# Kernel tuning notes

Measured on AMD Instinct MI355X. Metric: run time of the kernel, lower is better.

The kernel has to match this reference:

```python
import jax, jax.numpy as jnp
import numpy as np

N_NODES = 100000
HIDDEN = 128
N_ARCS = 1000000


def setup_inputs() -> dict:
    key = jax.random.key(0)
    k1, k2, k3, k4 = jax.random.split(key, 4)
    z = jax.random.normal(k1, (N_NODES, HIDDEN), dtype=jnp.float32)
    pot_arcs = jax.random.randint(k2, (N_ARCS, 2), 0, N_NODES, dtype=jnp.int64)
    # nn.Linear(2H, H): weight [H, 2H], bias [H]
    W1 = jax.random.normal(k3, (HIDDEN, 2 * HIDDEN), dtype=jnp.float32) * (1.0 / np.sqrt(2 * HIDDEN))
    b1 = jnp.zeros((HIDDEN,), dtype=jnp.float32)
    # nn.Linear(H, 1): weight [1, H], bias [1]
    W2 = jax.random.normal(k4, (1, HIDDEN), dtype=jnp.float32) * (1.0 / np.sqrt(HIDDEN))
    b2 = jnp.zeros((1,), dtype=jnp.float32)
    return {"z": z, "pot_arcs": pot_arcs, "W1": W1, "b1": b1, "W2": W2, "b2": b2}


def reference(z, pot_arcs, W1, b1, W2, b2):
    # Gather endpoint embeddings and concat: [E, 2H]
    h = jnp.concatenate([z[pot_arcs[:, 0]], z[pot_arcs[:, 1]]], axis=-1)
    h = jax.nn.relu(h @ W1.T + b1)        # [E, H]
    out = h @ W2.T + b2                   # [E, 1]
    return out.reshape(-1)                # [E]
```

## Files before the change

### kernel.cpp

```cpp
#include <hip/hip_runtime.h>
#include <hip/hip_bf16.h>

#define N_NODES 100000
#define NODES_PAD 100096
#define N_ARCS 1000000

typedef __attribute__((ext_vector_type(8))) short bf16x8;
typedef __attribute__((ext_vector_type(4))) float f32x4;

__device__ __forceinline__ unsigned pk2(float lo, float hi) {
    __hip_bfloat162 b = __float22bfloat162_rn(make_float2(lo, hi));
    union { __hip_bfloat162 b; unsigned u; } c; c.b = b; return c.u;
}

__device__ __forceinline__ uint4 pack8(const float4 a, const float4 b) {
    uint4 r;
    r.x = pk2(a.x, a.y);
    r.y = pk2(a.z, a.w);
    r.z = pk2(b.x, b.y);
    r.w = pk2(b.z, b.w);
    return r;
}

__global__ __launch_bounds__(256) void gemm_uv_q(const float* __restrict__ z,
                                                 const float* __restrict__ W1,
                                                 const float* __restrict__ b1,
                                                 unsigned char* __restrict__ UVq,
                                                 float* __restrict__ scl) {
    __shared__ unsigned short As[64 * 128];
    __shared__ unsigned short Bs[128 * 128];
    const int tid = threadIdx.x;
    const int y = blockIdx.y;
    const int c0 = y * 128;

    #pragma unroll
    for (int it = 0; it < 8; it++) {
        int i = tid + it * 256;
        int row = i >> 4, g = i & 15;
        const float4* s = (const float4*)(W1 + (long)row * 256 + c0 + g * 8);
        ((uint4*)Bs)[row * 16 + (g ^ (row & 15))] = pack8(s[0], s[1]);
    }

    const int lane = tid & 63;
    const int wave = tid >> 6;
    const int l16 = lane & 15;
    const int quad = lane >> 4;

    float bias[8];
    #pragma unroll
    for (int nt = 0; nt < 8; nt++)
        bias[nt] = (y == 0) ? b1[nt * 16 + l16] : 0.0f;

    float* sclh = scl + (long)y * NODES_PAD;

    for (int m0 = blockIdx.x * 64; m0 < N_NODES; m0 += gridDim.x * 64) {
        #pragma unroll
        for (int it = 0; it < 4; it++) {
            int i = tid + it * 256;
            int row = i >> 4, g = i & 15;
            int node = m0 + row;
            uint4 p = make_uint4(0u, 0u, 0u, 0u);
            if (node < N_NODES) {
                const float4* s = (const float4*)(z + (long)node * 128 + g * 8);
                p = pack8(s[0], s[1]);
            }
            ((uint4*)As)[row * 16 + (g ^ (row & 15))] = p;
        }
        __syncthreads();

        const int arow = wave * 16 + l16;
        f32x4 acc[8] = {};
        #pragma unroll
        for (int ks = 0; ks < 4; ks++) {
            const int gb = ks * 4 + quad;
            const bf16x8 a = *(const bf16x8*)&As[arow * 128 + ((gb ^ l16) << 3)];
            #pragma unroll
            for (int nt = 0; nt < 8; nt++) {
                const bf16x8 b = *(const bf16x8*)&Bs[(nt * 16 + l16) * 128 + ((gb ^ l16) << 3)];
                acc[nt] = __builtin_amdgcn_mfma_f32_16x16x32_bf16(a, b, acc[nt], 0, 0, 0);
            }
        }

        float m[4] = {0.f, 0.f, 0.f, 0.f};
        #pragma unroll
        for (int nt = 0; nt < 8; nt++)
            #pragma unroll
            for (int r = 0; r < 4; r++) {
                acc[nt][r] += bias[nt];
                m[r] = fmaxf(m[r], fabsf(acc[nt][r]));
            }
        #pragma unroll
        for (int o = 1; o <= 8; o <<= 1)
            #pragma unroll
            for (int r = 0; r < 4; r++)
                m[r] = fmaxf(m[r], __shfl_xor(m[r], o));

        const int rbase = m0 + wave * 16 + quad * 4;
        float inv[4];
        #pragma unroll
        for (int r = 0; r < 4; r++) {
            m[r] = fmaxf(m[r], 1e-30f);
            inv[r] = 127.0f * __builtin_amdgcn_rcpf(m[r]);
        }
        if (l16 == 0)
            *(float4*)(sclh + rbase) = make_float4(m[0] * (1.f / 127.f), m[1] * (1.f / 127.f),
                                                   m[2] * (1.f / 127.f), m[3] * (1.f / 127.f));
        #pragma unroll
        for (int r = 0; r < 4; r++) {
            unsigned lo = 0, hi = 0;
            #pragma unroll
            for (int nt = 0; nt < 4; nt++) {
                unsigned q = (unsigned)__float2int_rn(fmaf(acc[nt][r], inv[r], 128.f));
                lo |= (q & 0xffu) << (8 * nt);
            }
            #pragma unroll
            for (int nt = 4; nt < 8; nt++) {
                unsigned q = (unsigned)__float2int_rn(fmaf(acc[nt][r], inv[r], 128.f));
                hi |= (q & 0xffu) << (8 * (nt - 4));
            }
            *(uint2*)(UVq + (long)(rbase + r) * 256 + c0 + l16 * 8) = make_uint2(lo, hi);
        }
        __syncthreads();
    }
}

__global__ __launch_bounds__(256) void arc_score(const int4* __restrict__ arcs4,
                                                 const unsigned char* __restrict__ UVq,
                                                 const float* __restrict__ scl,
                                                 const float* __restrict__ W2,
                                                 const float* __restrict__ b2,
                                                 float* __restrict__ out) {
    const int tid = threadIdx.x;
    const int sub = tid & 7;
    const int gq = blockIdx.x * 32 + (tid >> 3);
    const int eb = sub * 16;

    float w2v[16], w2s = 0.f;
    #pragma unroll
    for (int i = 0; i < 16; i++) {
        int col = ((i & 7) << 4) + (sub << 1) + (i >> 3);
        w2v[i] = W2[col];
        w2s += w2v[i];
    }
    const float b2s = b2[0];
    const float* sclV = scl + NODES_PAD;

    const long stride = (long)gridDim.x * 64;
    const long limp = (long)(N_ARCS - 2) >> 1;

    long a = (long)gq * 2;
    int4 i0 = arcs4[a >> 1];
    uint4 u0 = *(const uint4*)(UVq + (long)i0.x * 256 + eb);
    uint4 v0 = *(const uint4*)(UVq + (long)i0.y * 256 + 128 + eb);
    uint4 u1 = *(const uint4*)(UVq + (long)i0.z * 256 + eb);
    uint4 v1 = *(const uint4*)(UVq + (long)i0.w * 256 + 128 + eb);
    float sU0 = scl[i0.x], sV0 = sclV[i0.y];
    float sU1 = scl[i0.z], sV1 = sclV[i0.w];
    long p1i = (a + stride) >> 1; if (p1i > limp) p1i = limp;
    int4 i1 = arcs4[p1i];

    while (true) {
        const long an = a + stride;
        uint4 nu0 = *(const uint4*)(UVq + (long)i1.x * 256 + eb);
        uint4 nv0 = *(const uint4*)(UVq + (long)i1.y * 256 + 128 + eb);
        uint4 nu1 = *(const uint4*)(UVq + (long)i1.z * 256 + eb);
        uint4 nv1 = *(const uint4*)(UVq + (long)i1.w * 256 + 128 + eb);
        float nsU0 = scl[i1.x], nsV0 = sclV[i1.y];
        float nsU1 = scl[i1.z], nsV1 = sclV[i1.w];
        long p2i = (an + stride) >> 1; if (p2i > limp) p2i = limp;
        int4 i2 = arcs4[p2i];

        const float r0 = sV0 * __builtin_amdgcn_rcpf(sU0);
        const float r1 = sV1 * __builtin_amdgcn_rcpf(sU1);
        const float C0 = fmaf(128.f, r0, 128.f);
        const float C1 = fmaf(128.f, r1, 128.f);

        float p0 = 0.f, p1 = 0.f;
        const unsigned* uw0 = (const unsigned*)&u0;
        const unsigned* vw0 = (const unsigned*)&v0;
        const unsigned* uw1 = (const unsigned*)&u1;
        const unsigned* vw1 = (const unsigned*)&v1;
        #pragma unroll
        for (int w = 0; w < 4; w++) {
            #pragma unroll
            for (int j = 0; j < 4; j++) {
                float gu0 = (float)((uw0[w] >> (8 * j)) & 0xffu);
                float gv0 = (float)((vw0[w] >> (8 * j)) & 0xffu);
                p0 = fmaf(fmaxf(fmaf(gv0, r0, gu0), C0), w2v[w * 4 + j], p0);
                float gu1 = (float)((uw1[w] >> (8 * j)) & 0xffu);
                float gv1 = (float)((vw1[w] >> (8 * j)) & 0xffu);
                p1 = fmaf(fmaxf(fmaf(gv1, r1, gu1), C1), w2v[w * 4 + j], p1);
            }
        }
        p0 = fmaf(-C0, w2s, p0);
        p1 = fmaf(-C1, w2s, p1);
        #pragma unroll
        for (int o = 4; o >= 1; o >>= 1) {
            p0 += __shfl_xor(p0, o);
            p1 += __shfl_xor(p1, o);
        }
        if (sub == 0) {
            out[a] = fmaf(sU0, p0, b2s);
            out[a + 1] = fmaf(sU1, p1, b2s);
        }

        if (an >= N_ARCS) break;
        a = an;
        u0 = nu0; v0 = nv0; u1 = nu1; v1 = nv1;
        sU0 = nsU0; sV0 = nsV0; sU1 = nsU1; sV1 = nsV1;
        i1 = i2;
    }
}

extern "C" void kernel_launch(void* const* d_in, const int* in_sizes, int n_in,
                              void* d_out, int out_size, void* d_ws, size_t ws_size,
                              hipStream_t stream) {
    const float* z  = (const float*)d_in[0];
    const int4* arcs4 = (const int4*)d_in[1];
    const float* W1 = (const float*)d_in[2];
    const float* b1 = (const float*)d_in[3];
    const float* W2 = (const float*)d_in[4];
    const float* b2 = (const float*)d_in[5];
    float* out = (float*)d_out;

    unsigned char* UVq = (unsigned char*)d_ws;
    float* scl = (float*)((char*)d_ws + (size_t)NODES_PAD * 256);

    hipLaunchKernelGGL(gemm_uv_q, dim3(384, 2), dim3(256), 0, stream,
                       z, W1, b1, UVq, scl);
    hipLaunchKernelGGL(arc_score, dim3(2048), dim3(256), 0, stream,
                       arcs4, UVq, scl, W2, b2, out);
}
```

Before: 145.0 us.

## Keep W1 tile in registers and double-buffer z tiles in GEMM kernel

The GEMM kernel now loads its B fragments (the W1 slice) once into registers, reusing that LDS space as the second A buffer. It also prefetches the next z tile into registers while the MFMAs for the current tile run, then writes it to the alternate LDS buffer. This hides global-load latency and removes repeated B reads from LDS in every iteration. The cost is heavy register pressure (32 bf16x8 B fragments plus 8 float4 prefetch registers), and launch_bounds asks for 2 blocks per CU, which could cause spills. Only the first kernel changes; the arc_score kernel, which likely dominates the time, is untouched.

Measured after the change: 151.9 us. 1.05x slower.

```diff
diff --git a/kernel.cpp b/kernel.cpp
--- a/kernel.cpp
+++ b/kernel.cpp
@@ -22,16 +22,24 @@
     return r;
 }
 
-__global__ __launch_bounds__(256) void gemm_uv_q(const float* __restrict__ z,
-                                                 const float* __restrict__ W1,
-                                                 const float* __restrict__ b1,
-                                                 unsigned char* __restrict__ UVq,
-                                                 float* __restrict__ scl) {
-    __shared__ unsigned short As[64 * 128];
-    __shared__ unsigned short Bs[128 * 128];
+__global__ __launch_bounds__(256, 2) void gemm_uv_q(const float* __restrict__ z,
+                                                    const float* __restrict__ W1,
+                                                    const float* __restrict__ b1,
+                                                    unsigned char* __restrict__ UVq,
+                                                    float* __restrict__ scl) {
+    __shared__ unsigned char lds[49152];
+    unsigned short* As0 = (unsigned short*)lds;
+    unsigned short* As1 = (unsigned short*)(lds + 16384);
+    unsigned short* Bs  = (unsigned short*)(lds + 16384);
+
     const int tid = threadIdx.x;
     const int y = blockIdx.y;
     const int c0 = y * 128;
+    const int lane = tid & 63;
+    const int wave = tid >> 6;
+    const int l16 = lane & 15;
+    const int quad = lane >> 4;
+    const int mstep = gridDim.x * 64;
 
     #pragma unroll
     for (int it = 0; it < 8; it++) {
@@ -40,44 +48,80 @@
         const float4* s = (const float4*)(W1 + (long)row * 256 + c0 + g * 8);
         ((uint4*)Bs)[row * 16 + (g ^ (row & 15))] = pack8(s[0], s[1]);
     }
-
-    const int lane = tid & 63;
-    const int wave = tid >> 6;
-    const int l16 = lane & 15;
-    const int quad = lane >> 4;
+    int m0 = blockIdx.x * 64;
+    #pragma unroll
+    for (int it = 0; it < 4; it++) {
+        int i = tid + it * 256;
+        int row = i >> 4, g = i & 15;
+        int node = m0 + row;
+        uint4 p = make_uint4(0u, 0u, 0u, 0u);
+        if (node < N_NODES) {
+            const float4* s = (const float4*)(z + (long)node * 128 + g * 8);
+            p = pack8(s[0], s[1]);
+        }
+        ((uint4*)As0)[row * 16 + (g ^ (row & 15))] = p;
+    }
+    __syncthreads();
+
+    bf16x8 breg[8][4];
+    #pragma unroll
+    for (int nt = 0; nt < 8; nt++)
+        #pragma unroll
+        for (int ks = 0; ks < 4; ks++)
+            breg[nt][ks] = *(const bf16x8*)&Bs[(nt * 16 + l16) * 128 +
+                                               (((ks * 4 + quad) ^ l16) << 3)];
+    __syncthreads();
 
     float bias[8];
     #pragma unroll
     for (int nt = 0; nt < 8; nt++)
         bias[nt] = (y == 0) ? b1[nt * 16 + l16] : 0.0f;
-
     float* sclh = scl + (long)y * NODES_PAD;
 
-    for (int m0 = blockIdx.x * 64; m0 < N_NODES; m0 += gridDim.x * 64) {
-        #pragma unroll
-        for (int it = 0; it < 4; it++) {
-            int i = tid + it * 256;
-            int row = i >> 4, g = i & 15;
-            int node = m0 + row;
-            uint4 p = make_uint4(0u, 0u, 0u, 0u);
-            if (node < N_NODES) {
-                const float4* s = (const float4*)(z + (long)node * 128 + g * 8);
-                p = pack8(s[0], s[1]);
-            }
-            ((uint4*)As)[row * 16 + (g ^ (row & 15))] = p;
-        }
-        __syncthreads();
+    int t = 0;
+    while (m0 < N_NODES) {
+        const int m1 = m0 + mstep;
+        unsigned short* cur = (t & 1) ? As1 : As0;
+        unsigned short* nxt = (t & 1) ? As0 : As1;
+        const bool have_next = m1 < N_NODES;
+
+        float4 ld[8];
+        if (have_next) {
+            #pragma unroll
+            for (int it = 0; it < 4; it++) {
+                int i = tid + it * 256;
+                int row = i >> 4, g = i & 15;
+                int node = m1 + row;
+                if (node < N_NODES) {
+                    const float4* s = (const float4*)(z + (long)node * 128 + g * 8);
+                    ld[it * 2] = s[0];
+                    ld[it * 2 + 1] = s[1];
+                } else {
+                    ld[it * 2] = make_float4(0.f, 0.f, 0.f, 0.f);
+                    ld[it * 2 + 1] = make_float4(0.f, 0.f, 0.f, 0.f);
+                }
+            }
+        }
 
         const int arow = wave * 16 + l16;
         f32x4 acc[8] = {};
         #pragma unroll
         for (int ks = 0; ks < 4; ks++) {
-            const int gb = ks * 4 + quad;
-            const bf16x8 a = *(const bf16x8*)&As[arow * 128 + ((gb ^ l16) << 3)];
-            #pragma unroll
-            for (int nt = 0; nt < 8; nt++) {
-                const bf16x8 b = *(const bf16x8*)&Bs[(nt * 16 + l16) * 128 + ((gb ^ l16) << 3)];
-                acc[nt] = __builtin_amdgcn_mfma_f32_16x16x32_bf16(a, b, acc[nt], 0, 0, 0);
+            const bf16x8 a = *(const bf16x8*)&cur[arow * 128 +
+                                                  (((ks * 4 + quad) ^ l16) << 3)];
+            #pragma unroll
+            for (int nt = 0; nt < 8; nt++)
+                acc[nt] = __builtin_amdgcn_mfma_f32_16x16x32_bf16(a, breg[nt][ks],
+                                                                  acc[nt], 0, 0, 0);
+        }
+
+        if (have_next) {
+            #pragma unroll
+            for (int it = 0; it < 4; it++) {
+                int i = tid + it * 256;
+                int row = i >> 4, g = i & 15;
+                ((uint4*)nxt)[row * 16 + (g ^ (row & 15))] =
+                    pack8(ld[it * 2], ld[it * 2 + 1]);
             }
         }
 
@@ -121,6 +165,8 @@
             *(uint2*)(UVq + (long)(rbase + r) * 256 + c0 + l16 * 8) = make_uint2(lo, hi);
         }
         __syncthreads();
+        m0 = m1;
+        t ^= 1;
     }
 }
 
```

## Prefetch next node tile into registers during MFMA in gemm_uv_q

Applied to the files above, without the earlier changes.

The GEMM+quantize kernel now issues global loads for the next 64-node tile of z into registers before running the MFMA loop on the current tile. It writes them to shared memory after the quantized output is stored. The aim is to hide global load latency behind compute and epilogue work. This costs 32 extra VGPRs for the prefetch buffer and adds a barrier, which may reduce occupancy. The grid of 384 blocks over about 1563 tiles gives each block only about four iterations, so there is little to overlap.

Result: no change. 145.0 us (median of 2 runs) (+0.0%).

```diff
diff --git a/kernel.cpp b/kernel.cpp
--- a/kernel.cpp
+++ b/kernel.cpp
@@ -32,6 +32,11 @@
     const int tid = threadIdx.x;
     const int y = blockIdx.y;
     const int c0 = y * 128;
+    const int lane = tid & 63;
+    const int wave = tid >> 6;
+    const int l16 = lane & 15;
+    const int quad = lane >> 4;
+    const int mstep = gridDim.x * 64;
 
     #pragma unroll
     for (int it = 0; it < 8; it++) {
@@ -40,33 +45,49 @@
         const float4* s = (const float4*)(W1 + (long)row * 256 + c0 + g * 8);
         ((uint4*)Bs)[row * 16 + (g ^ (row & 15))] = pack8(s[0], s[1]);
     }
-
-    const int lane = tid & 63;
-    const int wave = tid >> 6;
-    const int l16 = lane & 15;
-    const int quad = lane >> 4;
+    int m0 = blockIdx.x * 64;
+    #pragma unroll
+    for (int it = 0; it < 4; it++) {
+        int i = tid + it * 256;
+        int row = i >> 4, g = i & 15;
+        int node = m0 + row;
+        uint4 p = make_uint4(0u, 0u, 0u, 0u);
+        if (node < N_NODES) {
+            const float4* s = (const float4*)(z + (long)node * 128 + g * 8);
+            p = pack8(s[0], s[1]);
+        }
+        ((uint4*)As)[row * 16 + (g ^ (row & 15))] = p;
+    }
+    __syncthreads();
 
     float bias[8];
     #pragma unroll
     for (int nt = 0; nt < 8; nt++)
         bias[nt] = (y == 0) ? b1[nt * 16 + l16] : 0.0f;
-
     float* sclh = scl + (long)y * NODES_PAD;
 
-    for (int m0 = blockIdx.x * 64; m0 < N_NODES; m0 += gridDim.x * 64) {
-        #pragma unroll
-        for (int it = 0; it < 4; it++) {
-            int i = tid + it * 256;
-            int row = i >> 4, g = i & 15;
-            int node = m0 + row;
-            uint4 p = make_uint4(0u, 0u, 0u, 0u);
-            if (node < N_NODES) {
-                const float4* s = (const float4*)(z + (long)node * 128 + g * 8);
-                p = pack8(s[0], s[1]);
-            }
-            ((uint4*)As)[row * 16 + (g ^ (row & 15))] = p;
-        }
-        __syncthreads();
+    while (m0 < N_NODES) {
+        const int m1 = m0 + mstep;
+        const bool have_next = m1 < N_NODES;
+
+        float4 ld[8];
+        if (have_next) {
+            #pragma unroll
+            for (int it = 0; it < 4; it++) {
+                int i = tid + it * 256;
+                int row = i >> 4;
+                int g = i & 15;
+                int node = m1 + row;
+                if (node < N_NODES) {
+                    const float4* s = (const float4*)(z + (long)node * 128 + g * 8);
+                    ld[it * 2] = s[0];
+                    ld[it * 2 + 1] = s[1];
+                } else {
+                    ld[it * 2] = make_float4(0.f, 0.f, 0.f, 0.f);
+                    ld[it * 2 + 1] = make_float4(0.f, 0.f, 0.f, 0.f);
+                }
+            }
+        }
 
         const int arow = wave * 16 + l16;
         f32x4 acc[8] = {};
@@ -80,6 +101,7 @@
                 acc[nt] = __builtin_amdgcn_mfma_f32_16x16x32_bf16(a, b, acc[nt], 0, 0, 0);
             }
         }
+        __syncthreads();
 
         float m[4] = {0.f, 0.f, 0.f, 0.f};
         #pragma unroll
@@ -120,7 +142,18 @@
             }
             *(uint2*)(UVq + (long)(rbase + r) * 256 + c0 + l16 * 8) = make_uint2(lo, hi);
         }
+
+        if (have_next) {
+            #pragma unroll
+            for (int it = 0; it < 4; it++) {
+                int i = tid + it * 256;
+                int row = i >> 4, g = i & 15;
+                ((uint4*)As)[row * 16 + (g ^ (row & 15))] =
+                    pack8(ld[it * 2], ld[it * 2 + 1]);
+            }
+        }
         __syncthreads();
+        m0 = m1;
     }
 }
 
```
